# Performance work log

Measured on AMD Instinct MI355X. Metric: run time of the kernel, lower is better.

## Reference

```python
import jax, jax.numpy as jnp
import numpy as np

N = 10000      # nodes
E = 160000     # edges
G = 128        # graphs in batch
DIMS = [16, 32, 32]  # in_channels, then conv output dims
HID = 25       # edge-MLP hidden width
EPS = 1e-5     # batch-norm eps


def setup_inputs() -> dict:
    key = jax.random.key(0)
    ks = iter(jax.random.split(key, 40))
    inp = {}
    inp["x"] = jax.random.normal(next(ks), (N, DIMS[0]), dtype=jnp.float32)
    inp["edge_attr"] = jax.random.uniform(next(ks), (E, 3), dtype=jnp.float32)
    inp["edge_index"] = jax.random.randint(next(ks), (2, E), 0, N, dtype=jnp.int32)
    inp["batch"] = jnp.sort(jax.random.randint(next(ks), (N,), 0, G, dtype=jnp.int32))
    for i in range(2):
        din, dout = DIMS[i], DIMS[i + 1]
        inp[f"w1_{i}"] = jax.random.normal(next(ks), (3, HID), dtype=jnp.float32) * 0.3
        inp[f"b1_{i}"] = jnp.zeros((HID,), jnp.float32)
        inp[f"g_{i}"] = jnp.ones((HID,), jnp.float32)
        inp[f"be_{i}"] = jnp.zeros((HID,), jnp.float32)
        inp[f"w2_{i}"] = jax.random.normal(next(ks), (HID, din * dout), dtype=jnp.float32) * 0.05
        inp[f"b2_{i}"] = jnp.zeros((din * dout,), jnp.float32)
        inp[f"wr_{i}"] = jax.random.normal(next(ks), (din, dout), dtype=jnp.float32) * 0.1
        inp[f"bc_{i}"] = jnp.zeros((dout,), jnp.float32)
    inp["wfc"] = jax.random.normal(next(ks), (DIMS[-1], 1), dtype=jnp.float32) * 0.1
    inp["bfc"] = jnp.zeros((1,), jnp.float32)
    return inp


def _ecn(x, edge_attr, layers, wfc, bfc, edge_index, batch):
    src, dst = edge_index[0], edge_index[1]
    deg = jax.ops.segment_sum(jnp.ones((E,), x.dtype), dst, num_segments=N)
    deg = jnp.clip(deg, 1.0)[:, None]          # [N,1], PyG mean clamps count>=1
    for (w1, b1, g, be, w2, b2, wr, bc) in layers:
        # edge MLP: Linear(3,25) -> BatchNorm(batch stats) -> ReLU -> Linear(25, in*out)
        h = edge_attr @ w1 + b1                 # [E,25]
        mu = h.mean(axis=0)
        var = h.var(axis=0)
        h = (h - mu) * jax.lax.rsqrt(var + EPS) * g + be
        h = jax.nn.relu(h)
        w = (h @ w2 + b2).reshape(E, x.shape[1], -1)   # [E,in,out] per-edge weights
        msg = jnp.einsum('ei,eio->eo', x[src], w)      # gather + per-edge matmul
        agg = jax.ops.segment_sum(msg, dst, num_segments=N) / deg  # scatter-mean
        x = agg + x @ wr + bc                   # root transform + bias
        x = jax.nn.elu(x)
    # global mean pool over graphs
    gsum = jax.ops.segment_sum(x, batch, num_segments=G)
    gcnt = jnp.clip(jax.ops.segment_sum(jnp.ones((N,), x.dtype), batch, num_segments=G), 1.0)
    pooled = gsum / gcnt[:, None]               # [G, dims[-1]]
    return pooled @ wfc + bfc                   # fc MLP last layer is plain Linear


def reference(x, edge_attr, edge_index, batch,
              w1_0, b1_0, g_0, be_0, w2_0, b2_0, wr_0, bc_0,
              w1_1, b1_1, g_1, be_1, w2_1, b2_1, wr_1, bc_1,
              wfc, bfc):
    layers = [
        (w1_0, b1_0, g_0, be_0, w2_0, b2_0, wr_0, bc_0),
        (w1_1, b1_1, g_1, be_1, w2_1, b2_1, wr_1, bc_1),
    ]
    return _ecn(x, edge_attr, layers, wfc, bfc, edge_index, batch)
```

## Files before the change

kernel.cpp:

```cpp
#include <hip/hip_runtime.h>
#include <math.h>

#define NN   10000
#define EE   160000
#define GG   128
#define HIDK 25
#define KROWS 32
#define KB   28
#define DOUT 32
#define EPSBN 1e-5f
#define PREPB 1024
#define WPACKN (KROWS * 16 * DOUT + KROWS * 32 * DOUT)
#define MAXD 64

#define OFF_CUR   0
#define OFF_GSUM  10016
#define OFF_GMOM  14112
#define OFF_GCNT  14128
#define ZERO_FLOATS 14256
#define OFF_W1F0  14256
#define OFF_B1F0  14336
#define OFF_W1F1  14368
#define OFF_B1F1  14448
#define OFF_EA    14480
#define OFF_WB0   2574480
#define OFF_WB1   2590864
#define OFF_X1    2623632
#define TOTAL_FLOATS 2943632

__device__ inline float wave_red(float v) {
    for (int off = 32; off; off >>= 1) v += __shfl_down(v, off);
    return v;
}

template <int DIN>
__device__ inline void wpack(int idx, const float* __restrict__ w2,
                             const float* __restrict__ b2,
                             const float* __restrict__ wr,
                             const float* __restrict__ bc,
                             float* __restrict__ wbig) {
    int k = idx / (DIN * DOUT);
    int rem = idx - k * (DIN * DOUT);
    int i4 = rem / (4 * DOUT);
    int rem2 = rem - i4 * (4 * DOUT);
    int o = rem2 >> 2, c = rem2 & 3;
    int i = i4 * 4 + c;
    float v = 0.f;
    if (k < HIDK) v = w2[(k * DIN + i) * DOUT + o];
    else if (k == HIDK) v = b2[i * DOUT + o];
    else if (k == HIDK + 1) v = wr[i * DOUT + o];
    else if (k == HIDK + 2) v = (i == 0) ? bc[o] : 0.f;
    wbig[idx] = v;
}

__global__ void k_prep(const float* __restrict__ ea, const int* __restrict__ ei,
                       const int* __restrict__ batch,
                       const float* __restrict__ w2_0, const float* __restrict__ b2_0,
                       const float* __restrict__ wr_0, const float* __restrict__ bc_0,
                       const float* __restrict__ w2_1, const float* __restrict__ b2_1,
                       const float* __restrict__ wr_1, const float* __restrict__ bc_1,
                       float* __restrict__ gmom, int* __restrict__ cur,
                       int* __restrict__ gcnt, float* __restrict__ eab,
                       float* __restrict__ wb0, float* __restrict__ wb1) {
    __shared__ float ls[4][9];
    int t = threadIdx.x;
    int idx = blockIdx.x * 256 + t;

    if (idx < KROWS * 16 * DOUT) wpack<16>(idx, w2_0, b2_0, wr_0, bc_0, wb0);
    else if (idx < WPACKN) wpack<32>(idx - KROWS * 16 * DOUT, w2_1, b2_1, wr_1, bc_1, wb1);

    float s[9];
#pragma unroll
    for (int j = 0; j < 9; j++) s[j] = 0.f;
    if (idx < EE) {
        float a0 = ea[3 * idx], a1 = ea[3 * idx + 1], a2 = ea[3 * idx + 2];
        s[0] = a0; s[1] = a1; s[2] = a2;
        s[3] = a0 * a0; s[4] = a0 * a1; s[5] = a0 * a2;
        s[6] = a1 * a1; s[7] = a1 * a2; s[8] = a2 * a2;
        int d = ei[EE + idx];
        int pos = atomicAdd(cur + d, 1);
        if (pos < MAXD) {
            int slot = d * MAXD + pos;
            float4 av = { a0, a1, a2, __int_as_float(ei[idx]) };
            *(float4*)(eab + 4 * (size_t)slot) = av;
        }
    }
    if (idx < NN) atomicAdd(gcnt + batch[idx], 1);

    int w = t >> 6, lane = t & 63;
#pragma unroll
    for (int j = 0; j < 9; j++) {
        float r = wave_red(s[j]);
        if (lane == 0) ls[w][j] = r;
    }
    __syncthreads();
    if (t < 9 && blockIdx.x * 256 < EE)
        atomicAdd(gmom + t, ls[0][t] + ls[1][t] + ls[2][t] + ls[3][t]);
}

__global__ void k_fold(const float* __restrict__ gmom,
                       const float* __restrict__ w1_0, const float* __restrict__ b1_0,
                       const float* __restrict__ g_0, const float* __restrict__ be_0,
                       const float* __restrict__ w1_1, const float* __restrict__ b1_1,
                       const float* __restrict__ g_1, const float* __restrict__ be_1,
                       float* __restrict__ w1f0, float* __restrict__ b1f0,
                       float* __restrict__ w1f1, float* __restrict__ b1f1) {
    int t = threadIdx.x;
    int grp = t >> 5, j = t & 31;
    if (grp > 1 || j >= HIDK) return;
    const float* w1 = grp ? w1_1 : w1_0;
    const float* b1 = grp ? b1_1 : b1_0;
    const float* g  = grp ? g_1  : g_0;
    const float* be = grp ? be_1 : be_0;
    float* w1f = grp ? w1f1 : w1f0;
    float* b1f = grp ? b1f1 : b1f0;
    const float inv = 1.0f / (float)EE;
    float m0 = gmom[0] * inv, m1 = gmom[1] * inv, m2 = gmom[2] * inv;
    float c00 = gmom[3] * inv - m0 * m0, c01 = gmom[4] * inv - m0 * m1;
    float c02 = gmom[5] * inv - m0 * m2, c11 = gmom[6] * inv - m1 * m1;
    float c12 = gmom[7] * inv - m1 * m2, c22 = gmom[8] * inv - m2 * m2;
    float w0 = w1[j], wa = w1[25 + j], wb = w1[50 + j];
    float mean = m0 * w0 + m1 * wa + m2 * wb + b1[j];
    float var = w0 * w0 * c00 + wa * wa * c11 + wb * wb * c22
              + 2.f * (w0 * wa * c01 + w0 * wb * c02 + wa * wb * c12);
    float sc = g[j] * rsqrtf(var + EPSBN);
    w1f[j] = w0 * sc; w1f[25 + j] = wa * sc; w1f[50 + j] = wb * sc;
    b1f[j] = (b1[j] - mean) * sc + be[j];
}

template <int DIN, int KPL, bool FINAL>
__global__ __launch_bounds__(256, 6)
void k_fused(const int* __restrict__ cnt,
             const float* __restrict__ eab,
             const float* __restrict__ w1f, const float* __restrict__ b1f,
             const float* __restrict__ wbig, const float* __restrict__ xin,
             const int* __restrict__ batch,
             float* __restrict__ xout, float* __restrict__ gsum) {
    __shared__ __align__(16) float Slds[4][KROWS][DIN];
    __shared__ float Olds[4][4][DOUT];
    __shared__ __align__(16) float hb[4][2][2][32];
    int t = threadIdx.x;
    int w = t >> 6, lane = t & 63;
    int n = blockIdx.x * 4 + w;
    int dg = cnt[n];
    int start = n * MAXD;
    int end = start + (dg > MAXD ? MAXD : dg);

    int il = lane & (DIN - 1);
    int kh = lane / DIN;
    int kme = lane & 31;
    int half = lane >> 5;

    float c0 = 0.f, c1 = 0.f, c2 = 0.f, c3 = 0.f;
    if (kme < HIDK) {
        c0 = w1f[kme]; c1 = w1f[25 + kme]; c2 = w1f[50 + kme]; c3 = b1f[kme];
    } else if (kme == HIDK) {
        c3 = 1.0f;
    }

    float x_own = xin[n * DIN + il];

    float s[KPL];
#pragma unroll
    for (int j = 0; j < KPL; j++) s[j] = 0.f;

    const float4* ea4 = (const float4*)eab;

    int p = start;
    int vB0 = 0, vB1 = 0;
    float xA = 0.f, xB = 0.f;
    float4 av1 = {0.f, 0.f, 0.f, 0.f};
    int buf = 0;

    if (p < end) {
        vB0 = (p + 1 < end); int qB0 = vB0 ? p + 1 : p;
        float4 av0 = ea4[half ? qB0 : p];
        int p1 = p + 2;
        if (p1 < end) {
            vB1 = (p1 + 1 < end); int qB1 = vB1 ? p1 + 1 : p1;
            av1 = ea4[half ? qB1 : p1];
        }
        int me0 = __float_as_int(av0.w);
        int sA0 = __shfl(me0, 0), sB0 = __shfl(me0, 32);
        xA = xin[sA0 * DIN + il];
        xB = xin[sB0 * DIN + il];
        float hv = av0.x * c0 + av0.y * c1 + av0.z * c2 + c3;
        hv = hv > 0.f ? hv : 0.f;
        hb[w][0][half][kme] = hv;
    }
    while (p < end) {
        int p1 = p + 2, p2 = p + 4;
        float4 av2 = {0.f, 0.f, 0.f, 0.f};
        int vB2 = 0;
        if (p2 < end) {
            vB2 = (p2 + 1 < end); int qB2 = vB2 ? p2 + 1 : p2;
            av2 = ea4[half ? qB2 : p2];
        }
        int me1 = __float_as_int(av1.w);
        int sA1 = __shfl(me1, 0), sB1 = __shfl(me1, 32);
        float xAn = 0.f, xBn = 0.f;
        if (p1 < end) { xAn = xin[sA1 * DIN + il]; xBn = xin[sB1 * DIN + il]; }
        const float4* hA4 = (const float4*)&hb[w][buf][0][kh * KPL];
        const float4* hB4 = (const float4*)&hb[w][buf][1][kh * KPL];
        float4 ha[KPL / 4], hc[KPL / 4];
#pragma unroll
        for (int j4 = 0; j4 < KPL / 4; j4++) { ha[j4] = hA4[j4]; hc[j4] = hB4[j4]; }
        if (p1 < end) {
            float hv = av1.x * c0 + av1.y * c1 + av1.z * c2 + c3;
            hv = hv > 0.f ? hv : 0.f;
            hb[w][buf ^ 1][half][kme] = hv;
        }
        float xBm = vB0 ? xB : 0.f;
#pragma unroll
        for (int j4 = 0; j4 < KPL / 4; j4++) {
            s[j4 * 4 + 0] += ha[j4].x * xA; s[j4 * 4 + 1] += ha[j4].y * xA;
            s[j4 * 4 + 2] += ha[j4].z * xA; s[j4 * 4 + 3] += ha[j4].w * xA;
        }
#pragma unroll
        for (int j4 = 0; j4 < KPL / 4; j4++) {
            s[j4 * 4 + 0] += hc[j4].x * xBm; s[j4 * 4 + 1] += hc[j4].y * xBm;
            s[j4 * 4 + 2] += hc[j4].z * xBm; s[j4 * 4 + 3] += hc[j4].w * xBm;
        }
        p = p1;
        vB0 = vB1; vB1 = vB2;
        xA = xAn; xB = xBn; av1 = av2;
        buf ^= 1;
    }
#pragma unroll
    for (int j = 0; j < KPL; j++)
        Slds[w][kh * KPL + j][il] = s[j];
    float dmul = (float)dg; if (dmul < 1.f) dmul = 1.f;
    if (half == 0) {
        Slds[w][26][il] = dmul * x_own;
        Slds[w][27][il] = (il == 0) ? dmul : 0.f;
    }
    __syncthreads();

    {
        int o = lane & 31, hf = lane >> 5;
        constexpr int I4H = DIN / 8;
        const float4* wb4 = (const float4*)wbig;
        float a0 = 0.f, a1 = 0.f, a2 = 0.f, a3 = 0.f;
        int kbase = w * (KB / 4);
#pragma unroll
        for (int kk = 0; kk < KB / 4; kk++) {
            int k = kbase + kk;
#pragma unroll
            for (int j = 0; j < I4H; j++) {
                int i4 = hf * I4H + j;
                float4 wv = wb4[(k * (DIN / 4) + i4) * 32 + o];
                float4 s0 = *(const float4*)&Slds[0][k][i4 * 4];
                float4 s1 = *(const float4*)&Slds[1][k][i4 * 4];
                float4 s2 = *(const float4*)&Slds[2][k][i4 * 4];
                float4 s3 = *(const float4*)&Slds[3][k][i4 * 4];
                a0 += s0.x * wv.x + s0.y * wv.y + s0.z * wv.z + s0.w * wv.w;
                a1 += s1.x * wv.x + s1.y * wv.y + s1.z * wv.z + s1.w * wv.w;
                a2 += s2.x * wv.x + s2.y * wv.y + s2.z * wv.z + s2.w * wv.w;
                a3 += s3.x * wv.x + s3.y * wv.y + s3.z * wv.z + s3.w * wv.w;
            }
        }
        a0 += __shfl_xor(a0, 32);
        a1 += __shfl_xor(a1, 32);
        a2 += __shfl_xor(a2, 32);
        a3 += __shfl_xor(a3, 32);
        if (hf == 0) {
            Olds[w][0][o] = a0; Olds[w][1][o] = a1;
            Olds[w][2][o] = a2; Olds[w][3][o] = a3;
        }
    }
    __syncthreads();

    if (t < 4 * DOUT) {
        int m = t >> 5, o2 = t & 31;
        int n2 = blockIdx.x * 4 + m;
        float d = (float)cnt[n2]; if (d < 1.f) d = 1.f;
        float r = (Olds[0][m][o2] + Olds[1][m][o2] + Olds[2][m][o2] + Olds[3][m][o2]) / d;
        r = r > 0.f ? r : expm1f(r);
        if (FINAL) atomicAdd(gsum + batch[n2] * DOUT + o2, r);
        else xout[n2 * DOUT + o2] = r;
    }
}

__global__ void k_fc(const float* __restrict__ gsum, const int* __restrict__ gcnt,
                     const float* __restrict__ wfc, const float* __restrict__ bfc,
                     float* __restrict__ out) {
    int g = threadIdx.x;
    if (g >= GG) return;
    float c = (float)gcnt[g]; if (c < 1.f) c = 1.f;
    float acc = 0.f;
#pragma unroll
    for (int o = 0; o < DOUT; o++) acc += gsum[g * DOUT + o] * wfc[o];
    out[g] = acc / c + bfc[0];
}

extern "C" void kernel_launch(void* const* d_in, const int* in_sizes, int n_in,
                              void* d_out, int out_size, void* d_ws, size_t ws_size,
                              hipStream_t stream) {
    const float* x     = (const float*)d_in[0];
    const float* ea    = (const float*)d_in[1];
    const int*   ei    = (const int*)d_in[2];
    const int*   batch = (const int*)d_in[3];
    const float* w1_0 = (const float*)d_in[4];
    const float* b1_0 = (const float*)d_in[5];
    const float* g_0  = (const float*)d_in[6];
    const float* be_0 = (const float*)d_in[7];
    const float* w2_0 = (const float*)d_in[8];
    const float* b2_0 = (const float*)d_in[9];
    const float* wr_0 = (const float*)d_in[10];
    const float* bc_0 = (const float*)d_in[11];
    const float* w1_1 = (const float*)d_in[12];
    const float* b1_1 = (const float*)d_in[13];
    const float* g_1  = (const float*)d_in[14];
    const float* be_1 = (const float*)d_in[15];
    const float* w2_1 = (const float*)d_in[16];
    const float* b2_1 = (const float*)d_in[17];
    const float* wr_1 = (const float*)d_in[18];
    const float* bc_1 = (const float*)d_in[19];
    const float* wfc  = (const float*)d_in[20];
    const float* bfc  = (const float*)d_in[21];

    float* ws    = (float*)d_ws;
    int*   cur   = (int*)(ws + OFF_CUR);
    float* gsum  = ws + OFF_GSUM;
    float* gmom  = ws + OFF_GMOM;
    int*   gcnt  = (int*)(ws + OFF_GCNT);
    float* w1f0  = ws + OFF_W1F0;
    float* b1f0  = ws + OFF_B1F0;
    float* w1f1  = ws + OFF_W1F1;
    float* b1f1  = ws + OFF_B1F1;
    float* eab   = ws + OFF_EA;
    float* wb0   = ws + OFF_WB0;
    float* wb1   = ws + OFF_WB1;
    float* x1    = ws + OFF_X1;

    hipMemsetAsync(ws, 0, (size_t)ZERO_FLOATS * sizeof(float), stream);

    k_prep<<<PREPB, 256, 0, stream>>>(ea, ei, batch,
                                      w2_0, b2_0, wr_0, bc_0, w2_1, b2_1, wr_1, bc_1,
                                      gmom, cur, gcnt, eab, wb0, wb1);
    k_fold<<<1, 64, 0, stream>>>(gmom, w1_0, b1_0, g_0, be_0, w1_1, b1_1, g_1, be_1,
                                 w1f0, b1f0, w1f1, b1f1);

    k_fused<16, 8, false><<<NN / 4, 256, 0, stream>>>(cur, eab, w1f0, b1f0,
                                                      wb0, x, batch, x1, gsum);
    k_fused<32, 16, true><<<NN / 4, 256, 0, stream>>>(cur, eab, w1f1, b1f1,
                                                      wb1, x1, batch, nullptr, gsum);

    k_fc<<<1, 128, 0, stream>>>(gsum, gcnt, wfc, bfc, (float*)d_out);
}
```

Baseline: 193.7 us.

## Repack contraction weights per node-lane and replace moment atomics with per-block partials

The final contraction stage now assigns each lane one node and a pair of outputs (o, o+16), reading an interleaved weight layout with two float4 loads. This removes the cross-half shuffle reduction and the four-way LDS broadcast. Separately, the BN moment reduction no longer uses global float atomics on nine addresses; each prep block writes partial sums and k_fold reduces them with 256 threads. The trade-offs are more global weight loads per lane, a different LDS access pattern, and an extra partial-sum buffer.

```diff
diff --git a/kernel.cpp b/kernel.cpp
--- a/kernel.cpp
+++ b/kernel.cpp
@@ -15,18 +15,18 @@
 
 #define OFF_CUR   0
 #define OFF_GSUM  10016
-#define OFF_GMOM  14112
-#define OFF_GCNT  14128
-#define ZERO_FLOATS 14256
-#define OFF_W1F0  14256
-#define OFF_B1F0  14336
-#define OFF_W1F1  14368
-#define OFF_B1F1  14448
-#define OFF_EA    14480
-#define OFF_WB0   2574480
-#define OFF_WB1   2590864
-#define OFF_X1    2623632
-#define TOTAL_FLOATS 2943632
+#define OFF_GCNT  14112
+#define ZERO_FLOATS 14240
+#define OFF_MOP   14240
+#define OFF_W1F0  26528
+#define OFF_B1F0  26608
+#define OFF_W1F1  26640
+#define OFF_B1F1  26720
+#define OFF_EA    26752
+#define OFF_WB0   2586752
+#define OFF_WB1   2603136
+#define OFF_X1    2635904
+#define TOTAL_FLOATS 2955904
 
 __device__ inline float wave_red(float v) {
     for (int off = 32; off; off >>= 1) v += __shfl_down(v, off);
@@ -41,10 +41,12 @@
                              float* __restrict__ wbig) {
     int k = idx / (DIN * DOUT);
     int rem = idx - k * (DIN * DOUT);
-    int i4 = rem / (4 * DOUT);
-    int rem2 = rem - i4 * (4 * DOUT);
-    int o = rem2 >> 2, c = rem2 & 3;
+    int i4 = rem / 128;
+    int rem2 = rem - i4 * 128;
+    int o16 = rem2 >> 3, e = rem2 & 7;
+    int c = e >> 1, hi = e & 1;
     int i = i4 * 4 + c;
+    int o = o16 + hi * 16;
     float v = 0.f;
     if (k < HIDK) v = w2[(k * DIN + i) * DOUT + o];
     else if (k == HIDK) v = b2[i * DOUT + o];
@@ -59,7 +61,7 @@
                        const float* __restrict__ wr_0, const float* __restrict__ bc_0,
                        const float* __restrict__ w2_1, const float* __restrict__ b2_1,
                        const float* __restrict__ wr_1, const float* __restrict__ bc_1,
-                       float* __restrict__ gmom, int* __restrict__ cur,
+                       float* __restrict__ mop, int* __restrict__ cur,
                        int* __restrict__ gcnt, float* __restrict__ eab,
                        float* __restrict__ wb0, float* __restrict__ wb1) {
     __shared__ float ls[4][9];
@@ -94,38 +96,58 @@
         if (lane == 0) ls[w][j] = r;
     }
     __syncthreads();
-    if (t < 9 && blockIdx.x * 256 < EE)
-        atomicAdd(gmom + t, ls[0][t] + ls[1][t] + ls[2][t] + ls[3][t]);
-}
-
-__global__ void k_fold(const float* __restrict__ gmom,
+    if (t < 9) mop[blockIdx.x * 12 + t] = ls[0][t] + ls[1][t] + ls[2][t] + ls[3][t];
+}
+
+__global__ void k_fold(const float* __restrict__ mop,
                        const float* __restrict__ w1_0, const float* __restrict__ b1_0,
                        const float* __restrict__ g_0, const float* __restrict__ be_0,
                        const float* __restrict__ w1_1, const float* __restrict__ b1_1,
                        const float* __restrict__ g_1, const float* __restrict__ be_1,
                        float* __restrict__ w1f0, float* __restrict__ b1f0,
                        float* __restrict__ w1f1, float* __restrict__ b1f1) {
+    __shared__ float ls[4][9];
+    __shared__ float mo[9];
     int t = threadIdx.x;
-    int grp = t >> 5, j = t & 31;
-    if (grp > 1 || j >= HIDK) return;
-    const float* w1 = grp ? w1_1 : w1_0;
-    const float* b1 = grp ? b1_1 : b1_0;
-    const float* g  = grp ? g_1  : g_0;
-    const float* be = grp ? be_1 : be_0;
-    float* w1f = grp ? w1f1 : w1f0;
-    float* b1f = grp ? b1f1 : b1f0;
-    const float inv = 1.0f / (float)EE;
-    float m0 = gmom[0] * inv, m1 = gmom[1] * inv, m2 = gmom[2] * inv;
-    float c00 = gmom[3] * inv - m0 * m0, c01 = gmom[4] * inv - m0 * m1;
-    float c02 = gmom[5] * inv - m0 * m2, c11 = gmom[6] * inv - m1 * m1;
-    float c12 = gmom[7] * inv - m1 * m2, c22 = gmom[8] * inv - m2 * m2;
-    float w0 = w1[j], wa = w1[25 + j], wb = w1[50 + j];
-    float mean = m0 * w0 + m1 * wa + m2 * wb + b1[j];
-    float var = w0 * w0 * c00 + wa * wa * c11 + wb * wb * c22
-              + 2.f * (w0 * wa * c01 + w0 * wb * c02 + wa * wb * c12);
-    float sc = g[j] * rsqrtf(var + EPSBN);
-    w1f[j] = w0 * sc; w1f[25 + j] = wa * sc; w1f[50 + j] = wb * sc;
-    b1f[j] = (b1[j] - mean) * sc + be[j];
+    float s[9];
+#pragma unroll
+    for (int j = 0; j < 9; j++) s[j] = 0.f;
+    for (int b = t; b < PREPB; b += 256) {
+#pragma unroll
+        for (int j = 0; j < 9; j++) s[j] += mop[b * 12 + j];
+    }
+    int w = t >> 6, lane = t & 63;
+#pragma unroll
+    for (int j = 0; j < 9; j++) {
+        float r = wave_red(s[j]);
+        if (lane == 0) ls[w][j] = r;
+    }
+    __syncthreads();
+    if (t < 9) mo[t] = ls[0][t] + ls[1][t] + ls[2][t] + ls[3][t];
+    __syncthreads();
+    if (t < 64) {
+        int grp = t >> 5, j = t & 31;
+        if (j < HIDK) {
+            const float* w1 = grp ? w1_1 : w1_0;
+            const float* b1 = grp ? b1_1 : b1_0;
+            const float* g  = grp ? g_1  : g_0;
+            const float* be = grp ? be_1 : be_0;
+            float* w1f = grp ? w1f1 : w1f0;
+            float* b1f = grp ? b1f1 : b1f0;
+            const float inv = 1.0f / (float)EE;
+            float m0 = mo[0] * inv, m1 = mo[1] * inv, m2 = mo[2] * inv;
+            float c00 = mo[3] * inv - m0 * m0, c01 = mo[4] * inv - m0 * m1;
+            float c02 = mo[5] * inv - m0 * m2, c11 = mo[6] * inv - m1 * m1;
+            float c12 = mo[7] * inv - m1 * m2, c22 = mo[8] * inv - m2 * m2;
+            float w0 = w1[j], wa = w1[25 + j], wb = w1[50 + j];
+            float mean = m0 * w0 + m1 * wa + m2 * wb + b1[j];
+            float var = w0 * w0 * c00 + wa * wa * c11 + wb * wb * c22
+                      + 2.f * (w0 * wa * c01 + w0 * wb * c02 + wa * wb * c12);
+            float sc = g[j] * rsqrtf(var + EPSBN);
+            w1f[j] = w0 * sc; w1f[25 + j] = wa * sc; w1f[50 + j] = wb * sc;
+            b1f[j] = (b1[j] - mean) * sc + be[j];
+        }
+    }
 }
 
 template <int DIN, int KPL, bool FINAL>
@@ -237,36 +259,24 @@
     __syncthreads();
 
     {
-        int o = lane & 31, hf = lane >> 5;
-        constexpr int I4H = DIN / 8;
+        int o16 = lane & 15, nd = lane >> 4;
         const float4* wb4 = (const float4*)wbig;
-        float a0 = 0.f, a1 = 0.f, a2 = 0.f, a3 = 0.f;
+        float accO = 0.f, accP = 0.f;
         int kbase = w * (KB / 4);
 #pragma unroll
         for (int kk = 0; kk < KB / 4; kk++) {
             int k = kbase + kk;
 #pragma unroll
-            for (int j = 0; j < I4H; j++) {
-                int i4 = hf * I4H + j;
-                float4 wv = wb4[(k * (DIN / 4) + i4) * 32 + o];
-                float4 s0 = *(const float4*)&Slds[0][k][i4 * 4];
-                float4 s1 = *(const float4*)&Slds[1][k][i4 * 4];
-                float4 s2 = *(const float4*)&Slds[2][k][i4 * 4];
-                float4 s3 = *(const float4*)&Slds[3][k][i4 * 4];
-                a0 += s0.x * wv.x + s0.y * wv.y + s0.z * wv.z + s0.w * wv.w;
-                a1 += s1.x * wv.x + s1.y * wv.y + s1.z * wv.z + s1.w * wv.w;
-                a2 += s2.x * wv.x + s2.y * wv.y + s2.z * wv.z + s2.w * wv.w;
-                a3 += s3.x * wv.x + s3.y * wv.y + s3.z * wv.z + s3.w * wv.w;
+            for (int i4 = 0; i4 < DIN / 4; i4++) {
+                float4 sv = *(const float4*)&Slds[nd][k][i4 * 4];
+                const float4* wp = wb4 + ((size_t)(k * (DIN / 4) + i4) * 16 + o16) * 2;
+                float4 lo = wp[0], hi = wp[1];
+                accO += sv.x * lo.x + sv.y * lo.z + sv.z * hi.x + sv.w * hi.z;
+                accP += sv.x * lo.y + sv.y * lo.w + sv.z * hi.y + sv.w * hi.w;
             }
         }
-        a0 += __shfl_xor(a0, 32);
-        a1 += __shfl_xor(a1, 32);
-        a2 += __shfl_xor(a2, 32);
-        a3 += __shfl_xor(a3, 32);
-        if (hf == 0) {
-            Olds[w][0][o] = a0; Olds[w][1][o] = a1;
-            Olds[w][2][o] = a2; Olds[w][3][o] = a3;
-        }
+        Olds[w][nd][o16] = accO;
+        Olds[w][nd][o16 + 16] = accP;
     }
     __syncthreads();
 
@@ -322,8 +332,8 @@
     float* ws    = (float*)d_ws;
     int*   cur   = (int*)(ws + OFF_CUR);
     float* gsum  = ws + OFF_GSUM;
-    float* gmom  = ws + OFF_GMOM;
     int*   gcnt  = (int*)(ws + OFF_GCNT);
+    float* mop   = ws + OFF_MOP;
     float* w1f0  = ws + OFF_W1F0;
     float* b1f0  = ws + OFF_B1F0;
     float* w1f1  = ws + OFF_W1F1;
@@ -337,9 +347,9 @@
 
     k_prep<<<PREPB, 256, 0, stream>>>(ea, ei, batch,
                                       w2_0, b2_0, wr_0, bc_0, w2_1, b2_1, wr_1, bc_1,
-                                      gmom, cur, gcnt, eab, wb0, wb1);
-    k_fold<<<1, 64, 0, stream>>>(gmom, w1_0, b1_0, g_0, be_0, w1_1, b1_1, g_1, be_1,
-                                 w1f0, b1f0, w1f1, b1f1);
+                                      mop, cur, gcnt, eab, wb0, wb1);
+    k_fold<<<1, 256, 0, stream>>>(mop, w1_0, b1_0, g_0, be_0, w1_1, b1_1, g_1, be_1,
+                                  w1f0, b1f0, w1f1, b1f1);
 
     k_fused<16, 8, false><<<NN / 4, 256, 0, stream>>>(cur, eab, w1f0, b1f0,
                                                       wb0, x, batch, x1, gsum);
```

After: 216.3 us. +11.7%, slower.
